# Performance work log

Measured on AMD Instinct MI355X. Metric: run time of the kernel, lower is better.

Reference implementation:

```python
import jax, jax.numpy as jnp
import numpy as np

B, L, DIM, H, HD = 2, 2048, 1024, 16, 64


def _rope_tables(L, hd):
    inv_freq = 1.0 / (10000.0 ** (np.arange(0, hd, 2, dtype=np.float32) / hd))
    t = np.arange(L, dtype=np.float32)
    freqs = np.outer(t, inv_freq)                 # [L, hd/2]
    emb = np.concatenate([freqs, freqs], axis=-1)  # [L, hd]
    return jnp.asarray(np.cos(emb)), jnp.asarray(np.sin(emb))


def setup_inputs() -> dict:
    key = jax.random.key(0)
    k1, k2, k3 = jax.random.split(key, 3)
    x = jax.random.normal(k1, (B, L, DIM), dtype=jnp.float32)
    cos, sin = _rope_tables(L, HD)
    w_qkv = jax.random.normal(k2, (DIM, 3 * H * HD), dtype=jnp.float32) * (DIM ** -0.5)
    w_out = jax.random.normal(k3, (H * HD, DIM), dtype=jnp.float32) * ((H * HD) ** -0.5)
    return {"x": x, "cos": cos, "sin": sin, "w_qkv": w_qkv, "w_out": w_out}


def _rotate_half(u):
    u1, u2 = jnp.split(u, 2, axis=-1)
    return jnp.concatenate([-u2, u1], axis=-1)


def _apply_rope(u, cos, sin):
    # u: [B, L, H, hd]; cos/sin: [L, hd]
    c = cos[None, :, None, :]
    s = sin[None, :, None, :]
    return u * c + _rotate_half(u) * s


def reference(x, cos, sin, w_qkv, w_out):
    b, l, _ = x.shape
    qkv = jnp.einsum('bld,de->ble', x, w_qkv).reshape(b, l, 3 * H, HD)
    q, k, v = jnp.split(qkv, 3, axis=2)          # each [B, L, H, hd]
    q = _apply_rope(q, cos, sin)
    k = _apply_rope(k, cos, sin)
    scale = HD ** -0.5                            # SDPA default scale
    scores = jnp.einsum('bqhd,bkhd->bhqk', q, k) * scale
    attn = jax.nn.softmax(scores, axis=-1)
    o = jnp.einsum('bhqk,bkhd->bqhd', attn, v).reshape(b, l, H * HD)
    return jnp.einsum('ble,ed->bld', o, w_out)
```

## Files before the change

kernel.cpp:

```cpp
#include <hip/hip_runtime.h>
#include <hip/hip_bf16.h>

#define BATCH 2
#define SEQ   2048
#define DIM   1024
#define NH    16
#define HD    64
#define K_DIM 1024

typedef __attribute__((ext_vector_type(8))) short short8;
typedef __attribute__((ext_vector_type(4))) short short4v;
typedef __attribute__((ext_vector_type(4))) float f32x4;
typedef unsigned short ushort_t;

__device__ __forceinline__ unsigned short f2b(float x) {
    unsigned int u = __float_as_uint(x);
    u += 0x7FFFu + ((u >> 16) & 1u);
    return (unsigned short)(u >> 16);
}

#define ASYNC_COPY16(gp, lp) \
    __builtin_amdgcn_global_load_lds((const __attribute__((address_space(1))) void*)(gp), \
                                     (__attribute__((address_space(3))) void*)(lp), 16, 0, 0)

__global__ __launch_bounds__(256)
void prep(const float* __restrict__ x, const float* __restrict__ w_qkv,
          const float* __restrict__ w_out, ushort_t* __restrict__ xb,
          ushort_t* __restrict__ wqb, ushort_t* __restrict__ wob)
{
    const int bid = blockIdx.x;
    if (bid < 1024) {
        constexpr int n4 = (BATCH * SEQ * DIM) / 4;
        int i = bid * 256 + threadIdx.x;
        for (; i < n4; i += 1024 * 256) {
            float4 v = ((const float4*)x)[i];
            short4v o;
            o[0] = (short)f2b(v.x); o[1] = (short)f2b(v.y);
            o[2] = (short)f2b(v.z); o[3] = (short)f2b(v.w);
            ((short4v*)xb)[i] = o;
        }
    } else {
        const int lane = threadIdx.x & 63;
        const float* src; ushort_t* dst; int N, job;
        if (bid < 2560) { src = w_qkv; dst = wqb; N = 3072; job = (bid - 1024) * 4 + (threadIdx.x >> 6); }
        else            { src = w_out; dst = wob; N = 1024; job = (bid - 2560) * 4 + (threadIdx.x >> 6); }
        const int jn = (N == 3072) ? (job % 48) : (job % 16);
        const int jk = (N == 3072) ? (job / 48) : (job / 16);
        const int n  = jn * 64 + lane;
        const int k0 = jk * 8;
        short8 o;
        #pragma unroll
        for (int j = 0; j < 8; ++j) o[j] = (short)f2b(src[(size_t)(k0 + j) * N + n]);
        *(short8*)(dst + (size_t)n * K_DIM + k0) = o;
    }
}

__device__ __forceinline__ void gemm_stage(const ushort_t* __restrict__ Ag,
                                           const ushort_t* __restrict__ Bg,
                                           ushort_t* As, ushort_t* Bs,
                                           int k0, int w, int r0, int c0)
{
    ASYNC_COPY16(Ag + (size_t)r0 * K_DIM + k0 + c0 * 8,        As + w * 512);
    ASYNC_COPY16(Ag + (size_t)(64 + r0) * K_DIM + k0 + c0 * 8, As + w * 512 + 2048);
    ASYNC_COPY16(Bg + (size_t)r0 * K_DIM + k0 + c0 * 8,        Bs + w * 512);
    ASYNC_COPY16(Bg + (size_t)(64 + r0) * K_DIM + k0 + c0 * 8, Bs + w * 512 + 2048);
}

__device__ __forceinline__ void mfma_gemm_tile(
    const ushort_t* __restrict__ Ag, const ushort_t* __restrict__ Bg,
    ushort_t (&As)[2][128 * 32], ushort_t (&Bs)[2][128 * 32], f32x4 acc[4][4])
{
    const int t = threadIdx.x;
    const int w = t >> 6, lane = t & 63;
    const int qd = lane >> 4, cl = lane & 15;
    const int p0 = w * 64 + lane;
    const int r0 = p0 >> 2;
    const int c0 = (p0 & 3) ^ (r0 & 3);

    gemm_stage(Ag, Bg, As[0], Bs[0], 0, w, r0, c0);

    for (int kt = 0; kt < K_DIM / 32; ++kt) {
        const int cur = kt & 1;
        __syncthreads();
        if (kt + 1 < K_DIM / 32)
            gemm_stage(Ag, Bg, As[cur ^ 1], Bs[cur ^ 1], (kt + 1) * 32, w, r0, c0);

        short8 af[4], bfr[4];
        #pragma unroll
        for (int rt = 0; rt < 4; ++rt) {
            const int row = (w >> 1) * 64 + rt * 16 + cl;
            af[rt] = *(const short8*)(As[cur] + row * 32 + ((qd ^ (row & 3)) * 8));
        }
        #pragma unroll
        for (int ct = 0; ct < 4; ++ct) {
            const int col = (w & 1) * 64 + ct * 16 + cl;
            bfr[ct] = *(const short8*)(Bs[cur] + col * 32 + ((qd ^ (col & 3)) * 8));
        }
        #pragma unroll
        for (int rt = 0; rt < 4; ++rt)
            #pragma unroll
            for (int ct = 0; ct < 4; ++ct)
                acc[rt][ct] = __builtin_amdgcn_mfma_f32_16x16x32_bf16(
                    af[rt], bfr[ct], acc[rt][ct], 0, 0, 0);
    }
}

__global__ __launch_bounds__(256, 3)
void gemm_qkv_mfma(const ushort_t* __restrict__ xb, const ushort_t* __restrict__ wqb,
                   ushort_t* __restrict__ qb, ushort_t* __restrict__ kb,
                   ushort_t* __restrict__ vt,
                   const float* __restrict__ cosb, const float* __restrict__ sinb)
{
    __shared__ __align__(16) ushort_t As[2][128 * 32];
    __shared__ __align__(16) ushort_t Bs[2][128 * 32];
    const int m0 = blockIdx.y * 128, n0 = blockIdx.x * 128;

    f32x4 acc[4][4];
    #pragma unroll
    for (int i = 0; i < 4; ++i)
        #pragma unroll
        for (int j = 0; j < 4; ++j)
            #pragma unroll
            for (int r = 0; r < 4; ++r) acc[i][j][r] = 0.f;

    mfma_gemm_tile(xb + (size_t)m0 * K_DIM, wqb + (size_t)n0 * K_DIM, As, Bs, acc);

    const int t = threadIdx.x, w = t >> 6, lane = t & 63;
    const int qd = lane >> 4, cl = lane & 15;
    const int b = m0 >> 11;
    const int lbase = (m0 & 2047) + (w >> 1) * 64;
    const int region = blockIdx.x >> 3;
    const int h = (blockIdx.x & 7) * 2 + (w & 1);

    if (region < 2) {
        ushort_t* dst = region ? kb : qb;
        const float sc = region ? 1.0f : 0.18033688011111234f;
        #pragma unroll
        for (int rt = 0; rt < 4; ++rt) {
            #pragma unroll
            for (int r = 0; r < 4; ++r) {
                const int l = lbase + rt * 16 + qd * 4 + r;
                const float c0 = cosb[l * HD + cl],      s0 = sinb[l * HD + cl];
                const float c1 = cosb[l * HD + 16 + cl], s1 = sinb[l * HD + 16 + cl];
                const float v0 = acc[rt][0][r] * c0 - acc[rt][2][r] * s0;
                const float v1 = acc[rt][1][r] * c1 - acc[rt][3][r] * s1;
                const float v2 = acc[rt][2][r] * c0 + acc[rt][0][r] * s0;
                const float v3 = acc[rt][3][r] * c1 + acc[rt][1][r] * s1;
                short4v o4;
                o4[0] = (short)f2b(v0 * sc);
                o4[1] = (short)f2b(v1 * sc);
                o4[2] = (short)f2b(v2 * sc);
                o4[3] = (short)f2b(v3 * sc);
                *(short4v*)(dst + (((size_t)b * NH + h) * SEQ + l) * HD + cl * 4) = o4;
            }
        }
    } else {
        #pragma unroll
        for (int rt = 0; rt < 4; ++rt)
            #pragma unroll
            for (int ct = 0; ct < 4; ++ct) {
                const int d = ct * 16 + cl;
                const int l = lbase + rt * 16 + qd * 4;
                short4v o4;
                #pragma unroll
                for (int r = 0; r < 4; ++r) o4[r] = (short)f2b(acc[rt][ct][r]);
                *(short4v*)(vt + (((size_t)b * NH + h) * HD + d) * SEQ + l) = o4;
            }
    }
}

__device__ __forceinline__ void go_stage(const ushort_t* __restrict__ Ag,
                                         const ushort_t* __restrict__ Bg,
                                         ushort_t* As, ushort_t* Bs,
                                         int k0, int w, int lane)
{
    #pragma unroll
    for (int j = 0; j < 2; ++j) {
        const int r = w * 32 + j * 16 + (lane >> 2);
        const int c = (lane & 3) ^ (r & 3);
        ASYNC_COPY16(Ag + (size_t)r * K_DIM + k0 + c * 8, As + (w * 128 + j * 64) * 8);
    }
    const int rb = w * 16 + (lane >> 2);
    const int cb = (lane & 3) ^ (rb & 3);
    ASYNC_COPY16(Bg + (size_t)rb * K_DIM + k0 + cb * 8, Bs + (w * 64) * 8);
}

__global__ __launch_bounds__(256, 3)
void gemm_out_mfma(const ushort_t* __restrict__ ob, const ushort_t* __restrict__ wob,
                   float* __restrict__ out)
{
    __shared__ __align__(16) ushort_t As[2][128 * 32];
    __shared__ __align__(16) ushort_t Bs[2][64 * 32];
    const int m0 = blockIdx.y * 128, n0 = blockIdx.x * 64;
    const int t = threadIdx.x;
    const int w = t >> 6, lane = t & 63;
    const int qd = lane >> 4, cl = lane & 15;
    const int wr = w >> 1, wc = w & 1;

    f32x4 acc[4][2];
    #pragma unroll
    for (int i = 0; i < 4; ++i)
        #pragma unroll
        for (int j = 0; j < 2; ++j)
            #pragma unroll
            for (int r = 0; r < 4; ++r) acc[i][j][r] = 0.f;

    const ushort_t* Ag = ob  + (size_t)m0 * K_DIM;
    const ushort_t* Bg = wob + (size_t)n0 * K_DIM;
    go_stage(Ag, Bg, As[0], Bs[0], 0, w, lane);

    for (int kt = 0; kt < K_DIM / 32; ++kt) {
        const int cur = kt & 1;
        __syncthreads();
        if (kt + 1 < K_DIM / 32)
            go_stage(Ag, Bg, As[cur ^ 1], Bs[cur ^ 1], (kt + 1) * 32, w, lane);

        short8 af[4], bfr[2];
        #pragma unroll
        for (int rt = 0; rt < 4; ++rt) {
            const int row = wr * 64 + rt * 16 + cl;
            af[rt] = *(const short8*)(As[cur] + row * 32 + ((qd ^ (row & 3)) * 8));
        }
        #pragma unroll
        for (int ct = 0; ct < 2; ++ct) {
            const int col = wc * 32 + ct * 16 + cl;
            bfr[ct] = *(const short8*)(Bs[cur] + col * 32 + ((qd ^ (col & 3)) * 8));
        }
        #pragma unroll
        for (int rt = 0; rt < 4; ++rt)
            #pragma unroll
            for (int ct = 0; ct < 2; ++ct)
                acc[rt][ct] = __builtin_amdgcn_mfma_f32_16x16x32_bf16(
                    af[rt], bfr[ct], acc[rt][ct], 0, 0, 0);
    }

    const int mbase = m0 + wr * 64, nbase = n0 + wc * 32;
    #pragma unroll
    for (int rt = 0; rt < 4; ++rt)
        #pragma unroll
        for (int ct = 0; ct < 2; ++ct)
            #pragma unroll
            for (int r = 0; r < 4; ++r)
                out[(size_t)(mbase + rt * 16 + qd * 4 + r) * DIM + nbase + ct * 16 + cl] =
                    acc[rt][ct][r];
}

__global__ __launch_bounds__(256, 2)
void attn_mfma(const ushort_t* __restrict__ qb, const ushort_t* __restrict__ kb,
               const ushort_t* __restrict__ vt, ushort_t* __restrict__ ob)
{
    const int h = blockIdx.x;
    const int b = blockIdx.y;
    const int qt = blockIdx.z;
    const int t = threadIdx.x;
    const int w = t >> 6, lane = t & 63;
    const int qd = lane >> 4, cl = lane & 15;
    constexpr int NT = SEQ / 64;

    __shared__ __align__(16) ushort_t Ks[2][64 * 64];
    __shared__ __align__(16) ushort_t Vs[2][64 * 64];

    const size_t bh = (size_t)b * NH + h;
    const ushort_t* qbase = qb + (bh * SEQ + qt * 128 + w * 32) * HD;
    const ushort_t* kbase = kb + bh * SEQ * HD;
    const ushort_t* vbase = vt + bh * (size_t)HD * SEQ;

    const int p0 = w * 128 + lane;
    const int r0a = p0 >> 3,  c0a = (p0 & 7) ^ (r0a & 7);
    const int p1 = p0 + 64;
    const int r1a = p1 >> 3,  c1a = (p1 & 7) ^ (r1a & 7);
    const int ldsoff0 = (w * 128) * 8;
    const int ldsoff1 = (w * 128 + 64) * 8;

    short8 qf[2][2];
    #pragma unroll
    for (int nt = 0; nt < 2; ++nt)
        #pragma unroll
        for (int kh = 0; kh < 2; ++kh)
            qf[nt][kh] = *(const short8*)(qbase + (nt * 16 + cl) * HD + kh * 32 + qd * 8);

    f32x4 oaccT[4][2];
    float l_part[2] = {0.f, 0.f};
    #pragma unroll
    for (int dt = 0; dt < 4; ++dt)
        #pragma unroll
        for (int nt = 0; nt < 2; ++nt)
            #pragma unroll
            for (int r = 0; r < 4; ++r) oaccT[dt][nt][r] = 0.f;

    short8 pf_prev[2][2], vf_prev[4][2];
    #pragma unroll
    for (int nt = 0; nt < 2; ++nt)
        #pragma unroll
        for (int kh = 0; kh < 2; ++kh)
            #pragma unroll
            for (int e = 0; e < 8; ++e) pf_prev[nt][kh][e] = 0;
    #pragma unroll
    for (int dt = 0; dt < 4; ++dt)
        #pragma unroll
        for (int kh = 0; kh < 2; ++kh)
            #pragma unroll
            for (int e = 0; e < 8; ++e) vf_prev[dt][kh][e] = 0;

    {
        ASYNC_COPY16(kbase + (size_t)r0a * HD + c0a * 8,            (ushort_t*)Ks[0] + ldsoff0);
        ASYNC_COPY16(kbase + (size_t)r1a * HD + c1a * 8,            (ushort_t*)Ks[0] + ldsoff1);
        ASYNC_COPY16(vbase + (size_t)r0a * SEQ + c0a * 8,           (ushort_t*)Vs[0] + ldsoff0);
        ASYNC_COPY16(vbase + (size_t)r1a * SEQ + c1a * 8,           (ushort_t*)Vs[0] + ldsoff1);
    }

    for (int kt = 0; kt < NT; ++kt) {
        const int cur = kt & 1;
        __syncthreads();
        if (kt + 1 < NT) {
            const int g = kt + 1;
            ASYNC_COPY16(kbase + (size_t)(g * 64 + r0a) * HD + c0a * 8, (ushort_t*)Ks[cur ^ 1] + ldsoff0);
            ASYNC_COPY16(kbase + (size_t)(g * 64 + r1a) * HD + c1a * 8, (ushort_t*)Ks[cur ^ 1] + ldsoff1);
            ASYNC_COPY16(vbase + (size_t)r0a * SEQ + g * 64 + c0a * 8,  (ushort_t*)Vs[cur ^ 1] + ldsoff0);
            ASYNC_COPY16(vbase + (size_t)r1a * SEQ + g * 64 + c1a * 8,  (ushort_t*)Vs[cur ^ 1] + ldsoff1);
        }

        short8 kf[4][2], vf[4][2];
        #pragma unroll
        for (int mt = 0; mt < 4; ++mt)
            #pragma unroll
            for (int kh = 0; kh < 2; ++kh)
                kf[mt][kh] = *(const short8*)(Ks[cur] + ((mt * 16 + cl) * 8 + ((kh * 4 + qd) ^ (cl & 7))) * 8);
        #pragma unroll
        for (int dt = 0; dt < 4; ++dt)
            #pragma unroll
            for (int kh = 0; kh < 2; ++kh)
                vf[dt][kh] = *(const short8*)(Vs[cur] + ((dt * 16 + cl) * 8 + ((kh * 4 + qd) ^ (cl & 7))) * 8);

        f32x4 s[4][2];
        #pragma unroll
        for (int mt = 0; mt < 4; ++mt)
            #pragma unroll
            for (int nt = 0; nt < 2; ++nt)
                #pragma unroll
                for (int r = 0; r < 4; ++r) s[mt][nt][r] = 0.f;
        __builtin_amdgcn_s_setprio(1);
        #pragma unroll
        for (int kh = 0; kh < 2; ++kh)
            #pragma unroll
            for (int mt = 0; mt < 4; ++mt)
                #pragma unroll
                for (int nt = 0; nt < 2; ++nt)
                    s[mt][nt] = __builtin_amdgcn_mfma_f32_16x16x32_bf16(
                        kf[mt][kh], qf[nt][kh], s[mt][nt], 0, 0, 0);

        #pragma unroll
        for (int kh = 0; kh < 2; ++kh)
            #pragma unroll
            for (int dt = 0; dt < 4; ++dt)
                #pragma unroll
                for (int nt = 0; nt < 2; ++nt)
                    oaccT[dt][nt] = __builtin_amdgcn_mfma_f32_16x16x32_bf16(
                        vf_prev[dt][kh], pf_prev[nt][kh], oaccT[dt][nt], 0, 0, 0);
        __builtin_amdgcn_s_setprio(0);

        #pragma unroll
        for (int nt = 0; nt < 2; ++nt) {
            unsigned int wr[4][2];
            #pragma unroll
            for (int mt = 0; mt < 4; ++mt) {
                const float e0 = __builtin_amdgcn_exp2f(s[mt][nt][0]);
                const float e1 = __builtin_amdgcn_exp2f(s[mt][nt][1]);
                const float e2 = __builtin_amdgcn_exp2f(s[mt][nt][2]);
                const float e3 = __builtin_amdgcn_exp2f(s[mt][nt][3]);
                l_part[nt] += (e0 + e1) + (e2 + e3);
                union { __hip_bfloat162 h2; unsigned int u; } pk0, pk1;
                pk0.h2 = __float22bfloat162_rn(make_float2(e0, e1));
                pk1.h2 = __float22bfloat162_rn(make_float2(e2, e3));
                wr[mt][0] = pk0.u;
                wr[mt][1] = pk1.u;
            }
            #pragma unroll
            for (int kh = 0; kh < 2; ++kh) {
                union { unsigned int u[4]; short8 s8; } pu;
                #pragma unroll
                for (int i = 0; i < 2; ++i) {
                    unsigned int a  = wr[2 * kh][i];
                    unsigned int bb = wr[2 * kh + 1][i];
                    asm("v_permlane32_swap_b32 %0, %1" : "+v"(a), "+v"(bb));
                    asm("v_permlane16_swap_b32 %0, %1" : "+v"(a), "+v"(bb));
                    pu.u[i]     = a;
                    pu.u[2 + i] = bb;
                }
                pf_prev[nt][kh] = pu.s8;
            }
        }
        #pragma unroll
        for (int dt = 0; dt < 4; ++dt)
            #pragma unroll
            for (int kh = 0; kh < 2; ++kh)
                vf_prev[dt][kh] = vf[dt][kh];
    }

    #pragma unroll
    for (int kh = 0; kh < 2; ++kh)
        #pragma unroll
        for (int dt = 0; dt < 4; ++dt)
            #pragma unroll
            for (int nt = 0; nt < 2; ++nt)
                oaccT[dt][nt] = __builtin_amdgcn_mfma_f32_16x16x32_bf16(
                    vf_prev[dt][kh], pf_prev[nt][kh], oaccT[dt][nt], 0, 0, 0);

    #pragma unroll
    for (int nt = 0; nt < 2; ++nt) {
        float l = l_part[nt];
        l += __shfl_xor(l, 16);
        l += __shfl_xor(l, 32);
        const float inv = 1.0f / l;
        const int query = qt * 128 + w * 32 + nt * 16 + cl;
        ushort_t* op = ob + ((size_t)b * SEQ + query) * DIM + h * HD;
        #pragma unroll
        for (int dt = 0; dt < 4; ++dt) {
            short4v o4;
            #pragma unroll
            for (int r = 0; r < 4; ++r) o4[r] = (short)f2b(oaccT[dt][nt][r] * inv);
            *(short4v*)(op + dt * 16 + qd * 4) = o4;
        }
    }
}

extern "C" void kernel_launch(void* const* d_in, const int* in_sizes, int n_in,
                              void* d_out, int out_size, void* d_ws, size_t ws_size,
                              hipStream_t stream)
{
    const float* x     = (const float*)d_in[0];
    const float* cosb  = (const float*)d_in[1];
    const float* sinb  = (const float*)d_in[2];
    const float* w_qkv = (const float*)d_in[3];
    const float* w_out = (const float*)d_in[4];
    float* out = (float*)d_out;

    constexpr size_t MB = 1u << 20;
    char* ws = (char*)d_ws;
    ushort_t* qb  = (ushort_t*)(ws);
    ushort_t* kb  = (ushort_t*)(ws + 8 * MB);
    ushort_t* vt  = (ushort_t*)(ws + 16 * MB);
    ushort_t* wob = (ushort_t*)(ws + 24 * MB);
    ushort_t* ob  = (ushort_t*)(ws + 26 * MB);
    ushort_t* xb  = (ushort_t*)(ws + 34 * MB);
    ushort_t* wqb = (ushort_t*)(ws + 42 * MB);

    prep<<<3072, 256, 0, stream>>>(x, w_qkv, w_out, xb, wqb, wob);
    gemm_qkv_mfma<<<dim3(24, 32), 256, 0, stream>>>(xb, wqb, qb, kb, vt, cosb, sinb);
    attn_mfma<<<dim3(16, 2, 16), 256, 0, stream>>>(qb, kb, vt, ob);
    gemm_out_mfma<<<dim3(16, 32), 256, 0, stream>>>(ob, wob, out);
}
```

Before: 191.0 us.

## Unroll attention loop by two with ping-pong registers and MFMA row-sum

Unrolls the key-tile loop by two so LDS buffers and P/V register sets alternate statically. This removes the per-iteration register copies of V fragments and lets LDS addresses be precomputed pointers. The softmax denominator is now accumulated with an MFMA against a ones matrix, replacing the per-element VALU adds and cross-lane shuffles, and the score MFMAs start from a zero constant instead of a zeroed accumulator. It uses more registers, and the row sum is now taken over the bf16-rounded probabilities.

Measured after the change: 191.0 us. Within noise of the previous version (-0.0%).

```diff
diff --git a/kernel.cpp b/kernel.cpp
--- a/kernel.cpp
+++ b/kernel.cpp
@@ -272,6 +272,18 @@
     const int ldsoff0 = (w * 128) * 8;
     const int ldsoff1 = (w * 128 + 64) * 8;
 
+    const ushort_t* kg0 = kbase + (size_t)r0a * HD + c0a * 8;
+    const ushort_t* kg1 = kbase + (size_t)r1a * HD + c1a * 8;
+    const ushort_t* vg0 = vbase + (size_t)r0a * SEQ + c0a * 8;
+    const ushort_t* vg1 = vbase + (size_t)r1a * SEQ + c1a * 8;
+
+    const int lo0 = (cl * 8 + (qd ^ (cl & 7))) * 8;
+    const int lo1 = (cl * 8 + ((4 + qd) ^ (cl & 7))) * 8;
+    const ushort_t* kE0 = Ks[0] + lo0; const ushort_t* kE1 = Ks[0] + lo1;
+    const ushort_t* vE0 = Vs[0] + lo0; const ushort_t* vE1 = Vs[0] + lo1;
+    const ushort_t* kO0 = Ks[1] + lo0; const ushort_t* kO1 = Ks[1] + lo1;
+    const ushort_t* vO0 = Vs[1] + lo0; const ushort_t* vO1 = Vs[1] + lo1;
+
     short8 qf[2][2];
     #pragma unroll
     for (int nt = 0; nt < 2; ++nt)
@@ -279,122 +291,208 @@
         for (int kh = 0; kh < 2; ++kh)
             qf[nt][kh] = *(const short8*)(qbase + (nt * 16 + cl) * HD + kh * 32 + qd * 8);
 
+    const f32x4 fz = {0.f, 0.f, 0.f, 0.f};
+    short8 onesA;
+    #pragma unroll
+    for (int e = 0; e < 8; ++e) onesA[e] = (short)0x3F80;
+
     f32x4 oaccT[4][2];
-    float l_part[2] = {0.f, 0.f};
+    f32x4 lacc[2];
     #pragma unroll
     for (int dt = 0; dt < 4; ++dt)
         #pragma unroll
         for (int nt = 0; nt < 2; ++nt)
             #pragma unroll
             for (int r = 0; r < 4; ++r) oaccT[dt][nt][r] = 0.f;
-
-    short8 pf_prev[2][2], vf_prev[4][2];
     #pragma unroll
     for (int nt = 0; nt < 2; ++nt)
         #pragma unroll
+        for (int r = 0; r < 4; ++r) lacc[nt][r] = 0.f;
+
+    short8 pfE[2][2], vfE[4][2], pfO[2][2], vfO[4][2];
+    #pragma unroll
+    for (int nt = 0; nt < 2; ++nt)
+        #pragma unroll
         for (int kh = 0; kh < 2; ++kh)
             #pragma unroll
-            for (int e = 0; e < 8; ++e) pf_prev[nt][kh][e] = 0;
+            for (int e = 0; e < 8; ++e) pfO[nt][kh][e] = 0;
     #pragma unroll
     for (int dt = 0; dt < 4; ++dt)
         #pragma unroll
         for (int kh = 0; kh < 2; ++kh)
             #pragma unroll
-            for (int e = 0; e < 8; ++e) vf_prev[dt][kh][e] = 0;
+            for (int e = 0; e < 8; ++e) vfO[dt][kh][e] = 0;
 
     {
-        ASYNC_COPY16(kbase + (size_t)r0a * HD + c0a * 8,            (ushort_t*)Ks[0] + ldsoff0);
-        ASYNC_COPY16(kbase + (size_t)r1a * HD + c1a * 8,            (ushort_t*)Ks[0] + ldsoff1);
-        ASYNC_COPY16(vbase + (size_t)r0a * SEQ + c0a * 8,           (ushort_t*)Vs[0] + ldsoff0);
-        ASYNC_COPY16(vbase + (size_t)r1a * SEQ + c1a * 8,           (ushort_t*)Vs[0] + ldsoff1);
-    }
-
-    for (int kt = 0; kt < NT; ++kt) {
-        const int cur = kt & 1;
+        ASYNC_COPY16(kg0, (ushort_t*)Ks[0] + ldsoff0);
+        ASYNC_COPY16(kg1, (ushort_t*)Ks[0] + ldsoff1);
+        ASYNC_COPY16(vg0, (ushort_t*)Vs[0] + ldsoff0);
+        ASYNC_COPY16(vg1, (ushort_t*)Vs[0] + ldsoff1);
+        kg0 += 64 * HD; kg1 += 64 * HD; vg0 += 64; vg1 += 64;
+    }
+
+    for (int pr = 0; pr < NT / 2; ++pr) {
         __syncthreads();
-        if (kt + 1 < NT) {
-            const int g = kt + 1;
-            ASYNC_COPY16(kbase + (size_t)(g * 64 + r0a) * HD + c0a * 8, (ushort_t*)Ks[cur ^ 1] + ldsoff0);
-            ASYNC_COPY16(kbase + (size_t)(g * 64 + r1a) * HD + c1a * 8, (ushort_t*)Ks[cur ^ 1] + ldsoff1);
-            ASYNC_COPY16(vbase + (size_t)r0a * SEQ + g * 64 + c0a * 8,  (ushort_t*)Vs[cur ^ 1] + ldsoff0);
-            ASYNC_COPY16(vbase + (size_t)r1a * SEQ + g * 64 + c1a * 8,  (ushort_t*)Vs[cur ^ 1] + ldsoff1);
-        }
-
-        short8 kf[4][2], vf[4][2];
-        #pragma unroll
-        for (int mt = 0; mt < 4; ++mt)
-            #pragma unroll
-            for (int kh = 0; kh < 2; ++kh)
-                kf[mt][kh] = *(const short8*)(Ks[cur] + ((mt * 16 + cl) * 8 + ((kh * 4 + qd) ^ (cl & 7))) * 8);
-        #pragma unroll
-        for (int dt = 0; dt < 4; ++dt)
-            #pragma unroll
-            for (int kh = 0; kh < 2; ++kh)
-                vf[dt][kh] = *(const short8*)(Vs[cur] + ((dt * 16 + cl) * 8 + ((kh * 4 + qd) ^ (cl & 7))) * 8);
-
-        f32x4 s[4][2];
-        #pragma unroll
-        for (int mt = 0; mt < 4; ++mt)
-            #pragma unroll
-            for (int nt = 0; nt < 2; ++nt)
-                #pragma unroll
-                for (int r = 0; r < 4; ++r) s[mt][nt][r] = 0.f;
-        __builtin_amdgcn_s_setprio(1);
-        #pragma unroll
-        for (int kh = 0; kh < 2; ++kh)
+        {
+            ASYNC_COPY16(kg0, (ushort_t*)Ks[1] + ldsoff0);
+            ASYNC_COPY16(kg1, (ushort_t*)Ks[1] + ldsoff1);
+            ASYNC_COPY16(vg0, (ushort_t*)Vs[1] + ldsoff0);
+            ASYNC_COPY16(vg1, (ushort_t*)Vs[1] + ldsoff1);
+            kg0 += 64 * HD; kg1 += 64 * HD; vg0 += 64; vg1 += 64;
+        }
+        {
+            short8 kf[4][2];
+            #pragma unroll
+            for (int mt = 0; mt < 4; ++mt) {
+                kf[mt][0] = *(const short8*)(kE0 + mt * 1024);
+                kf[mt][1] = *(const short8*)(kE1 + mt * 1024);
+            }
+            #pragma unroll
+            for (int dt = 0; dt < 4; ++dt) {
+                vfE[dt][0] = *(const short8*)(vE0 + dt * 1024);
+                vfE[dt][1] = *(const short8*)(vE1 + dt * 1024);
+            }
+            f32x4 s[4][2];
+            __builtin_amdgcn_s_setprio(1);
             #pragma unroll
             for (int mt = 0; mt < 4; ++mt)
                 #pragma unroll
                 for (int nt = 0; nt < 2; ++nt)
                     s[mt][nt] = __builtin_amdgcn_mfma_f32_16x16x32_bf16(
-                        kf[mt][kh], qf[nt][kh], s[mt][nt], 0, 0, 0);
-
-        #pragma unroll
-        for (int kh = 0; kh < 2; ++kh)
-            #pragma unroll
-            for (int dt = 0; dt < 4; ++dt)
+                        kf[mt][0], qf[nt][0], fz, 0, 0, 0);
+            #pragma unroll
+            for (int mt = 0; mt < 4; ++mt)
                 #pragma unroll
                 for (int nt = 0; nt < 2; ++nt)
-                    oaccT[dt][nt] = __builtin_amdgcn_mfma_f32_16x16x32_bf16(
-                        vf_prev[dt][kh], pf_prev[nt][kh], oaccT[dt][nt], 0, 0, 0);
-        __builtin_amdgcn_s_setprio(0);
-
-        #pragma unroll
-        for (int nt = 0; nt < 2; ++nt) {
-            unsigned int wr[4][2];
+                    s[mt][nt] = __builtin_amdgcn_mfma_f32_16x16x32_bf16(
+                        kf[mt][1], qf[nt][1], s[mt][nt], 0, 0, 0);
+            #pragma unroll
+            for (int kh = 0; kh < 2; ++kh)
+                #pragma unroll
+                for (int dt = 0; dt < 4; ++dt)
+                    #pragma unroll
+                    for (int nt = 0; nt < 2; ++nt)
+                        oaccT[dt][nt] = __builtin_amdgcn_mfma_f32_16x16x32_bf16(
+                            vfO[dt][kh], pfO[nt][kh], oaccT[dt][nt], 0, 0, 0);
+            __builtin_amdgcn_s_setprio(0);
+            #pragma unroll
+            for (int nt = 0; nt < 2; ++nt) {
+                unsigned int wr2[4][2];
+                #pragma unroll
+                for (int mt = 0; mt < 4; ++mt) {
+                    const float e0 = __builtin_amdgcn_exp2f(s[mt][nt][0]);
+                    const float e1 = __builtin_amdgcn_exp2f(s[mt][nt][1]);
+                    const float e2 = __builtin_amdgcn_exp2f(s[mt][nt][2]);
+                    const float e3 = __builtin_amdgcn_exp2f(s[mt][nt][3]);
+                    union { __hip_bfloat162 h2; unsigned int u; } pk0, pk1;
+                    pk0.h2 = __float22bfloat162_rn(make_float2(e0, e1));
+                    pk1.h2 = __float22bfloat162_rn(make_float2(e2, e3));
+                    wr2[mt][0] = pk0.u;
+                    wr2[mt][1] = pk1.u;
+                }
+                #pragma unroll
+                for (int kh = 0; kh < 2; ++kh) {
+                    union { unsigned int u[4]; short8 s8; } pu;
+                    #pragma unroll
+                    for (int i = 0; i < 2; ++i) {
+                        unsigned int a  = wr2[2 * kh][i];
+                        unsigned int bb = wr2[2 * kh + 1][i];
+                        asm("v_permlane32_swap_b32 %0, %1" : "+v"(a), "+v"(bb));
+                        asm("v_permlane16_swap_b32 %0, %1" : "+v"(a), "+v"(bb));
+                        pu.u[i]     = a;
+                        pu.u[2 + i] = bb;
+                    }
+                    pfE[nt][kh] = pu.s8;
+                }
+            }
+            #pragma unroll
+            for (int kh = 0; kh < 2; ++kh)
+                #pragma unroll
+                for (int nt = 0; nt < 2; ++nt)
+                    lacc[nt] = __builtin_amdgcn_mfma_f32_16x16x32_bf16(
+                        onesA, pfE[nt][kh], lacc[nt], 0, 0, 0);
+        }
+
+        __syncthreads();
+        if (pr + 1 < NT / 2) {
+            ASYNC_COPY16(kg0, (ushort_t*)Ks[0] + ldsoff0);
+            ASYNC_COPY16(kg1, (ushort_t*)Ks[0] + ldsoff1);
+            ASYNC_COPY16(vg0, (ushort_t*)Vs[0] + ldsoff0);
+            ASYNC_COPY16(vg1, (ushort_t*)Vs[0] + ldsoff1);
+            kg0 += 64 * HD; kg1 += 64 * HD; vg0 += 64; vg1 += 64;
+        }
+        {
+            short8 kf[4][2];
             #pragma unroll
             for (int mt = 0; mt < 4; ++mt) {
-                const float e0 = __builtin_amdgcn_exp2f(s[mt][nt][0]);
-                const float e1 = __builtin_amdgcn_exp2f(s[mt][nt][1]);
-                const float e2 = __builtin_amdgcn_exp2f(s[mt][nt][2]);
-                const float e3 = __builtin_amdgcn_exp2f(s[mt][nt][3]);
-                l_part[nt] += (e0 + e1) + (e2 + e3);
-                union { __hip_bfloat162 h2; unsigned int u; } pk0, pk1;
-                pk0.h2 = __float22bfloat162_rn(make_float2(e0, e1));
-                pk1.h2 = __float22bfloat162_rn(make_float2(e2, e3));
-                wr[mt][0] = pk0.u;
-                wr[mt][1] = pk1.u;
-            }
-            #pragma unroll
-            for (int kh = 0; kh < 2; ++kh) {
-                union { unsigned int u[4]; short8 s8; } pu;
-                #pragma unroll
-                for (int i = 0; i < 2; ++i) {
-                    unsigned int a  = wr[2 * kh][i];
-                    unsigned int bb = wr[2 * kh + 1][i];
-                    asm("v_permlane32_swap_b32 %0, %1" : "+v"(a), "+v"(bb));
-                    asm("v_permlane16_swap_b32 %0, %1" : "+v"(a), "+v"(bb));
-                    pu.u[i]     = a;
-                    pu.u[2 + i] = bb;
+                kf[mt][0] = *(const short8*)(kO0 + mt * 1024);
+                kf[mt][1] = *(const short8*)(kO1 + mt * 1024);
+            }
+            #pragma unroll
+            for (int dt = 0; dt < 4; ++dt) {
+                vfO[dt][0] = *(const short8*)(vO0 + dt * 1024);
+                vfO[dt][1] = *(const short8*)(vO1 + dt * 1024);
+            }
+            f32x4 s[4][2];
+            __builtin_amdgcn_s_setprio(1);
+            #pragma unroll
+            for (int mt = 0; mt < 4; ++mt)
+                #pragma unroll
+                for (int nt = 0; nt < 2; ++nt)
+                    s[mt][nt] = __builtin_amdgcn_mfma_f32_16x16x32_bf16(
+                        kf[mt][0], qf[nt][0], fz, 0, 0, 0);
+            #pragma unroll
+            for (int mt = 0; mt < 4; ++mt)
+                #pragma unroll
+                for (int nt = 0; nt < 2; ++nt)
+                    s[mt][nt] = __builtin_amdgcn_mfma_f32_16x16x32_bf16(
+                        kf[mt][1], qf[nt][1], s[mt][nt], 0, 0, 0);
+            #pragma unroll
+            for (int kh = 0; kh < 2; ++kh)
+                #pragma unroll
+                for (int dt = 0; dt < 4; ++dt)
+                    #pragma unroll
+                    for (int nt = 0; nt < 2; ++nt)
+                        oaccT[dt][nt] = __builtin_amdgcn_mfma_f32_16x16x32_bf16(
+                            vfE[dt][kh], pfE[nt][kh], oaccT[dt][nt], 0, 0, 0);
+            __builtin_amdgcn_s_setprio(0);
+            #pragma unroll
+            for (int nt = 0; nt < 2; ++nt) {
+                unsigned int wr2[4][2];
+                #pragma unroll
+                for (int mt = 0; mt < 4; ++mt) {
+                    const float e0 = __builtin_amdgcn_exp2f(s[mt][nt][0]);
+                    const float e1 = __builtin_amdgcn_exp2f(s[mt][nt][1]);
+                    const float e2 = __builtin_amdgcn_exp2f(s[mt][nt][2]);
+                    const float e3 = __builtin_amdgcn_exp2f(s[mt][nt][3]);
+                    union { __hip_bfloat162 h2; unsigned int u; } pk0, pk1;
+                    pk0.h2 = __float22bfloat162_rn(make_float2(e0, e1));
+                    pk1.h2 = __float22bfloat162_rn(make_float2(e2, e3));
+                    wr2[mt][0] = pk0.u;
+                    wr2[mt][1] = pk1.u;
                 }
-                pf_prev[nt][kh] = pu.s8;
-            }
-        }
-        #pragma unroll
-        for (int dt = 0; dt < 4; ++dt)
+                #pragma unroll
+                for (int kh = 0; kh < 2; ++kh) {
+                    union { unsigned int u[4]; short8 s8; } pu;
+                    #pragma unroll
+                    for (int i = 0; i < 2; ++i) {
+                        unsigned int a  = wr2[2 * kh][i];
+                        unsigned int bb = wr2[2 * kh + 1][i];
+                        asm("v_permlane32_swap_b32 %0, %1" : "+v"(a), "+v"(bb));
+                        asm("v_permlane16_swap_b32 %0, %1" : "+v"(a), "+v"(bb));
+                        pu.u[i]     = a;
+                        pu.u[2 + i] = bb;
+                    }
+                    pfO[nt][kh] = pu.s8;
+                }
+            }
             #pragma unroll
             for (int kh = 0; kh < 2; ++kh)
-                vf_prev[dt][kh] = vf[dt][kh];
+                #pragma unroll
+                for (int nt = 0; nt < 2; ++nt)
+                    lacc[nt] = __builtin_amdgcn_mfma_f32_16x16x32_bf16(
+                        onesA, pfO[nt][kh], lacc[nt], 0, 0, 0);
+        }
     }
 
     #pragma unroll
@@ -404,14 +502,11 @@
             #pragma unroll
             for (int nt = 0; nt < 2; ++nt)
                 oaccT[dt][nt] = __builtin_amdgcn_mfma_f32_16x16x32_bf16(
-                    vf_prev[dt][kh], pf_prev[nt][kh], oaccT[dt][nt], 0, 0, 0);
+                    vfO[dt][kh], pfO[nt][kh], oaccT[dt][nt], 0, 0, 0);
 
     #pragma unroll
     for (int nt = 0; nt < 2; ++nt) {
-        float l = l_part[nt];
-        l += __shfl_xor(l, 16);
-        l += __shfl_xor(l, 32);
-        const float inv = 1.0f / l;
+        const float inv = 1.0f / lacc[nt][0];
         const int query = qt * 128 + w * 32 + nt * 16 + cl;
         ushort_t* op = ob + ((size_t)b * SEQ + query) * DIM + h * HD;
         #pragma unroll
```
